# Optimization experiments

Hardware: AMD Instinct MI355X
Metric: run time of the kernel (lower is better)

## Reference

```python
import jax, jax.numpy as jnp
import numpy as np

LOG2 = float(np.log(2.0))

def ssp(x):
    # shifted softplus: softplus(x) - log(2)
    return jax.nn.softplus(x) - LOG2

def setup_inputs() -> dict:
    key = jax.random.key(0)
    ks = jax.random.split(key, 12)
    B, N, K, G, Fdim, H, O = 2, 1024, 64, 64, 128, 4, 128
    s = 0.05
    return {
        'x': jax.random.normal(ks[0], (B, N, Fdim), jnp.float32),
        'r_ij': jax.random.uniform(ks[1], (B, N, K), jnp.float32),
        'neighbors': jax.random.randint(ks[2], (B, N, K), 0, N),
        'pairwise_mask': jnp.ones((B, N, K), jnp.float32),
        'f_ij': jax.random.normal(ks[3], (B, N, K, G), jnp.float32),
        'w_in2f': jax.random.normal(ks[4], (H, Fdim, Fdim), jnp.float32) * s,
        'w_att': jax.random.normal(ks[5], (H, 2 * Fdim), jnp.float32) * s,
        'wf1': jax.random.normal(ks[6], (G, Fdim), jnp.float32) * s,
        'bf1': jnp.zeros((Fdim,), jnp.float32),
        'wf2': jax.random.normal(ks[7], (Fdim, Fdim), jnp.float32) * s,
        'bf2': jnp.zeros((Fdim,), jnp.float32),
        'w_out': jax.random.normal(ks[8], (Fdim, O), jnp.float32) * s,
        'b_out': jnp.zeros((O,), jnp.float32),
    }

def reference(x, r_ij, neighbors, pairwise_mask, f_ij,
              w_in2f, w_att, wf1, bf1, wf2, bf2, w_out, b_out):
    B, N, K = neighbors.shape
    H, _, Fdim = w_in2f.shape
    # continuous filter network: MLP on radial features -> [B,N,K,F]
    W = ssp(jnp.einsum('bnkg,gf->bnkf', f_ij, wf1) + bf1)
    W = jnp.einsum('bnkf,fe->bnke', W, wf2) + bf2
    # per-head linear projections: [B,H,N,F]
    y = jnp.einsum('bni,hif->bhnf', x, w_in2f)
    # gather neighbor features along atom axis: [B,H,N,K,F]
    idx = jnp.broadcast_to(neighbors.reshape(B, 1, N * K, 1), (B, H, N * K, Fdim))
    y_nb = jnp.take_along_axis(y, idx, axis=2).reshape(B, H, N, K, Fdim)
    # GAT attention logits via split weight (equiv. to concat + Dense):
    a_c = jnp.einsum('bhnf,hf->bhn', y, w_att[:, :Fdim])       # center part
    a_n = jnp.einsum('bhnkf,hf->bhnk', y_nb, w_att[:, Fdim:])  # neighbor part
    att = a_c[:, :, :, None] + a_n                             # [B,H,N,K]
    alpha = jax.nn.softmax(ssp(att), axis=-1)
    # attention-weighted neighbor features times continuous filters, mean over heads
    out = jnp.einsum('bhnk,bhnkf,bnkf->bnkf', alpha, y_nb, W) / H
    # masked aggregation over the neighbor axis
    agg = jnp.sum(out * pairwise_mask[..., None], axis=2)      # [B,N,F]
    return ssp(jnp.einsum('bnf,fo->bno', agg, w_out) + b_out)
```

## Files before the change

### kernel.cpp

```cpp
#include <hip/hip_runtime.h>

#define NB 2
#define NN 1024
#define NK 64
#define NG 64
#define NF 128
#define NH 4
#define NO 128
#define PITCH 132

typedef unsigned short ushort_t;
typedef __attribute__((ext_vector_type(8))) short short8v;
typedef __attribute__((ext_vector_type(4))) float f32x4;

union FragU { uint4 u4; short8v s8; };

__device__ __forceinline__ float bf2f(ushort_t u) {
    union { unsigned int i; float f; } v; v.i = ((unsigned int)u) << 16; return v.f;
}
__device__ __forceinline__ ushort_t f2bf(float f) {
    unsigned int u = __float_as_uint(f);
    unsigned int r = 0x7fffu + ((u >> 16) & 1u);
    return (ushort_t)((u + r) >> 16);
}
__device__ __forceinline__ float sspf(float x) {
    const float u = __builtin_amdgcn_exp2f(-fabsf(x) * 1.44269504088896341f);
    return fmaxf(x, 0.f) + fmaf(0.69314718055994531f,
                                __builtin_amdgcn_logf(1.f + u),
                                -0.69314718055994531f);
}

__global__ __launch_bounds__(256) void k_projprep(
    const float* __restrict__ x,
    const float* __restrict__ w_in2f,
    const float* __restrict__ w_att,
    const float* __restrict__ wf1, const float* __restrict__ wf2,
    const float* __restrict__ w_out,
    ushort_t* __restrict__ y,
    float* __restrict__ a_c,
    float* __restrict__ a_n,
    ushort_t* __restrict__ wf1f, ushort_t* __restrict__ wf2f,
    float* __restrict__ w_outT)
{
    const int t = threadIdx.x;
    __shared__ float xs[8][NF];
    __shared__ float ys[32][PITCH];

    if (blockIdx.x >= 256) {
        int s = (blockIdx.x - 256) * 256 + t;
        if (s >= 7168) return;
        if (s >= 3072) {
            const int s2 = s - 3072;
            const int o = s2 >> 5, fb = s2 & 31;
            #pragma unroll
            for (int j = 0; j < 4; ++j)
                w_outT[(size_t)o * NF + fb * 4 + j] = w_out[(size_t)(fb * 4 + j) * NO + o];
            return;
        }
        const float* W; ushort_t* out; int loOff;
        if (s < 1024) { W = wf1; out = wf1f; loOff = 8192; }
        else          { s -= 1024; W = wf2; out = wf2f; loOff = 16384; }
        const int fi = s >> 6, lane = s & 63;
        const int ks = fi >> 3, nf = fi & 7;
        const int n = nf * 16 + (lane & 15);
        const int kb = ks * 32 + ((lane >> 4) & 3) * 4;
        #pragma unroll
        for (int j = 0; j < 8; ++j) {
            const int k = kb + (j & 3) + ((j >> 2) << 4);
            const float v = W[(size_t)k * NF + n];
            const ushort_t hb = f2bf(v);
            out[(size_t)(fi * 64 + lane) * 8 + j] = hb;
            out[(size_t)loOff + (fi * 64 + lane) * 8 + j] = f2bf(v - bf2f(hb));
        }
        return;
    }

    const int bn0 = blockIdx.x * 8;
    {
        const float4* src = (const float4*)(x + (size_t)bn0 * NF);
        float4* dst = (float4*)(&xs[0][0]);
        dst[t] = src[t];
    }
    __syncthreads();

    const int hp = t >> 7;
    const int f0 = t & 127;
    const int h0 = hp, h1 = hp + 2;
    const float* w0 = w_in2f + (size_t)h0 * NF * NF + f0;
    const float* w1 = w_in2f + (size_t)h1 * NF * NF + f0;
    float acc0[8], acc1[8];
    #pragma unroll
    for (int n = 0; n < 8; ++n) { acc0[n] = 0.f; acc1[n] = 0.f; }

    for (int i0 = 0; i0 < NF; i0 += 4) {
        float4 xv[8];
        #pragma unroll
        for (int n = 0; n < 8; ++n) xv[n] = *(const float4*)&xs[n][i0];
        #pragma unroll
        for (int ii = 0; ii < 4; ++ii) {
            const float wa = w0[(size_t)(i0 + ii) * NF];
            const float wb = w1[(size_t)(i0 + ii) * NF];
            #pragma unroll
            for (int n = 0; n < 8; ++n) {
                const float xi = (&xv[n].x)[ii];
                acc0[n] = fmaf(xi, wa, acc0[n]);
                acc1[n] = fmaf(xi, wb, acc1[n]);
            }
        }
    }
    #pragma unroll
    for (int n = 0; n < 8; ++n) {
        const int bn = bn0 + n;
        const int b = bn >> 10, nn = bn & (NN - 1);
        y[((size_t)(b * NH + h0) * NN + nn) * NF + f0] = f2bf(acc0[n]);
        y[((size_t)(b * NH + h1) * NN + nn) * NF + f0] = f2bf(acc1[n]);
        ys[n * 4 + h0][f0] = acc0[n];
        ys[n * 4 + h1][f0] = acc1[n];
    }
    __syncthreads();

    {
        const int hn = t >> 3, q = t & 7;
        const int h = hn & 3, n = hn >> 2;
        float pc = 0.f, pn = 0.f;
        #pragma unroll
        for (int j = 0; j < 16; ++j) {
            const int f = q + 8 * j;
            const float yv = ys[n * 4 + h][f];
            pc = fmaf(yv, w_att[h * 2 * NF + f], pc);
            pn = fmaf(yv, w_att[h * 2 * NF + NF + f], pn);
        }
        #pragma unroll
        for (int off = 1; off < 8; off <<= 1) {
            pc += __shfl_xor(pc, off, 8);
            pn += __shfl_xor(pn, off, 8);
        }
        if (q == 0) {
            const int bn = bn0 + n;
            const int b = bn >> 10, nn = bn & (NN - 1);
            a_c[(size_t)(b * NH + h) * NN + nn] = pc;
            a_n[(size_t)(b * NH + h) * NN + nn] = pn;
        }
    }
}

__global__ __launch_bounds__(256, 7) void k_main(
    const int*      __restrict__ neighbors,
    const float*    __restrict__ pmask,
    const float*    __restrict__ f_ij,
    const float*    __restrict__ bf1,
    const float*    __restrict__ bf2v,
    const float*    __restrict__ w_outT,
    const float*    __restrict__ b_out,
    const ushort_t* __restrict__ y,
    const float*    __restrict__ a_c,
    const float*    __restrict__ a_n,
    const ushort_t* __restrict__ wf1f,
    const ushort_t* __restrict__ wf2f,
    float*          __restrict__ outp)
{
    const int bn = blockIdx.x;
    const int b = bn >> 10, n_ = bn & (NN - 1);
    const int t = threadIdx.x;

    __shared__ __align__(16) char smem[22784];
    ushort_t* fijs = (ushort_t*)(smem);
    ushort_t* W1   = (ushort_t*)(smem);
    ushort_t* W2   = (ushort_t*)(smem);
    float*    aggp = (float*)(smem + 16896);
    float*    aggc = (float*)(smem + 20992);
    float*    alpha = (float*)(smem + 21504);
    int*      nbs   = (int*)(smem + 22528);

    const int wave = t >> 6, lane = t & 63;
    const int lrow = lane & 15;
    const int lq   = (lane >> 4) & 3;
    const int wb   = wave * 32;

    {
        const float4* src = (const float4*)(f_ij + (size_t)bn * NK * NG);
        #pragma unroll
        for (int i = 0; i < 4; ++i) {
            const int e4 = i * 256 + t;
            const float4 v = src[e4];
            const int e = e4 * 4;
            const int row = e >> 6, col = e & 63;
            uint2 ph;
            ph.x = (unsigned)f2bf(v.x) | ((unsigned)f2bf(v.y) << 16);
            ph.y = (unsigned)f2bf(v.z) | ((unsigned)f2bf(v.w) << 16);
            *(uint2*)&fijs[row * 68 + col] = ph;
        }
    }
    if (t < NK) nbs[t] = neighbors[(size_t)bn * NK + t];
    __syncthreads();

    const float avc = a_c[(size_t)(b * NH + wave) * NN + n_];
    const float avn = a_n[(size_t)(b * NH + wave) * NN + nbs[lane]];
    const float pmk = pmask[(size_t)bn * NK + lane];

    f32x4 acc[4][2];
    {
        #pragma unroll
        for (int mf = 0; mf < 4; ++mf)
            #pragma unroll
            for (int nf2 = 0; nf2 < 2; ++nf2) acc[mf][nf2] = (f32x4)0.f;

        #pragma unroll
        for (int ks = 0; ks < 2; ++ks) {
            FragU b1h[2], b1l[2];
            #pragma unroll
            for (int nf2 = 0; nf2 < 2; ++nf2) {
                const int fi = ks * 8 + wave * 2 + nf2;
                b1h[nf2].u4 = *((const uint4*)wf1f + fi * 64 + lane);
                b1l[nf2].u4 = *((const uint4*)(wf1f + 8192) + fi * 64 + lane);
            }
            const int cb = ks * 32 + lq * 4;
            #pragma unroll
            for (int mf = 0; mf < 4; ++mf) {
                const int row = mf * 16 + lrow;
                FragU ah;
                {
                    const uint2 p0 = *(const uint2*)&fijs[row * 68 + cb];
                    const uint2 p1 = *(const uint2*)&fijs[row * 68 + cb + 16];
                    uint4 q; q.x = p0.x; q.y = p0.y; q.z = p1.x; q.w = p1.y; ah.u4 = q;
                }
                #pragma unroll
                for (int nf2 = 0; nf2 < 2; ++nf2) {
                    acc[mf][nf2] = __builtin_amdgcn_mfma_f32_16x16x32_bf16(ah.s8, b1h[nf2].s8, acc[mf][nf2], 0, 0, 0);
                    acc[mf][nf2] = __builtin_amdgcn_mfma_f32_16x16x32_bf16(ah.s8, b1l[nf2].s8, acc[mf][nf2], 0, 0, 0);
                }
            }
        }
    }
    __syncthreads();
    {
        const float bia[2] = { bf1[wb + lrow], bf1[wb + 16 + lrow] };
        #pragma unroll
        for (int mf = 0; mf < 4; ++mf)
            #pragma unroll
            for (int nf2 = 0; nf2 < 2; ++nf2) {
                const int col = wb + nf2 * 16 + lrow;
                #pragma unroll
                for (int r = 0; r < 4; ++r) {
                    const int row = mf * 16 + lq * 4 + r;
                    W1[row * 132 + col] = f2bf(sspf(acc[mf][nf2][r] + bia[nf2]));
                }
            }
    }
    __syncthreads();

    {
        #pragma unroll
        for (int mf = 0; mf < 4; ++mf)
            #pragma unroll
            for (int nf2 = 0; nf2 < 2; ++nf2) acc[mf][nf2] = (f32x4)0.f;

        for (int ks = 0; ks < 4; ++ks) {
            FragU b2h[2];
            #pragma unroll
            for (int nf2 = 0; nf2 < 2; ++nf2) {
                const int fi = ks * 8 + wave * 2 + nf2;
                b2h[nf2].u4 = *((const uint4*)wf2f + fi * 64 + lane);
            }
            const int cb = ks * 32 + lq * 4;
            #pragma unroll
            for (int mf = 0; mf < 4; ++mf) {
                const int row = mf * 16 + lrow;
                FragU ah;
                {
                    const uint2 p0 = *(const uint2*)&W1[row * 132 + cb];
                    const uint2 p1 = *(const uint2*)&W1[row * 132 + cb + 16];
                    uint4 q; q.x = p0.x; q.y = p0.y; q.z = p1.x; q.w = p1.y; ah.u4 = q;
                }
                #pragma unroll
                for (int nf2 = 0; nf2 < 2; ++nf2)
                    acc[mf][nf2] = __builtin_amdgcn_mfma_f32_16x16x32_bf16(ah.s8, b2h[nf2].s8, acc[mf][nf2], 0, 0, 0);
            }
        }
    }
    __syncthreads();
    {
        const float bia[2] = { bf2v[wb + lrow], bf2v[wb + 16 + lrow] };
        #pragma unroll
        for (int mf = 0; mf < 4; ++mf)
            #pragma unroll
            for (int nf2 = 0; nf2 < 2; ++nf2) {
                const int col = wb + nf2 * 16 + lrow;
                #pragma unroll
                for (int r = 0; r < 4; ++r) {
                    const int row = mf * 16 + lq * 4 + r;
                    W2[row * 132 + col] = f2bf(acc[mf][nf2][r] + bia[nf2]);
                }
            }
    }

    {
        const float att = sspf(avc + avn);
        float m = att;
        #pragma unroll
        for (int off = 32; off > 0; off >>= 1) m = fmaxf(m, __shfl_xor(m, off, 64));
        const float e = __builtin_amdgcn_exp2f((att - m) * 1.44269504088896341f);
        float s = e;
        #pragma unroll
        for (int off = 32; off > 0; off >>= 1) s += __shfl_xor(s, off, 64);
        alpha[wave * 64 + lane] = (e / s) * pmk;
    }
    __syncthreads();

    {
        const int fq = (t & 31) * 4;
        const int kg = t >> 5;
        float4 accv; accv.x = accv.y = accv.z = accv.w = 0.f;
        const ushort_t* yb = y + (size_t)b * NH * NN * NF;
        #pragma unroll 2
        for (int kk = 0; kk < 8; ++kk) {
            const int k = kg * 8 + kk;
            const int nb = nbs[k];
            const ushort_t* yp = yb + (size_t)nb * NF + fq;
            const uint2 u0 = *(const uint2*)(yp);
            const uint2 u1 = *(const uint2*)(yp + (size_t)NN * NF);
            const uint2 u2 = *(const uint2*)(yp + 2 * (size_t)NN * NF);
            const uint2 u3 = *(const uint2*)(yp + 3 * (size_t)NN * NF);
            const float a0 = alpha[0 * 64 + k], a1 = alpha[1 * 64 + k];
            const float a2 = alpha[2 * 64 + k], a3 = alpha[3 * 64 + k];
            float4 s;
            s.x = fmaf(a3, bf2f((ushort_t)(u3.x & 0xffffu)),
                  fmaf(a2, bf2f((ushort_t)(u2.x & 0xffffu)),
                  fmaf(a1, bf2f((ushort_t)(u1.x & 0xffffu)),
                       a0 * bf2f((ushort_t)(u0.x & 0xffffu)))));
            s.y = fmaf(a3, bf2f((ushort_t)(u3.x >> 16)),
                  fmaf(a2, bf2f((ushort_t)(u2.x >> 16)),
                  fmaf(a1, bf2f((ushort_t)(u1.x >> 16)),
                       a0 * bf2f((ushort_t)(u0.x >> 16)))));
            s.z = fmaf(a3, bf2f((ushort_t)(u3.y & 0xffffu)),
                  fmaf(a2, bf2f((ushort_t)(u2.y & 0xffffu)),
                  fmaf(a1, bf2f((ushort_t)(u1.y & 0xffffu)),
                       a0 * bf2f((ushort_t)(u0.y & 0xffffu)))));
            s.w = fmaf(a3, bf2f((ushort_t)(u3.y >> 16)),
                  fmaf(a2, bf2f((ushort_t)(u2.y >> 16)),
                  fmaf(a1, bf2f((ushort_t)(u1.y >> 16)),
                       a0 * bf2f((ushort_t)(u0.y >> 16)))));
            const uint2 wv = *(const uint2*)&W2[k * 132 + fq];
            accv.x = fmaf(bf2f((ushort_t)(wv.x & 0xffffu)), s.x, accv.x);
            accv.y = fmaf(bf2f((ushort_t)(wv.x >> 16)),     s.y, accv.y);
            accv.z = fmaf(bf2f((ushort_t)(wv.y & 0xffffu)), s.z, accv.z);
            accv.w = fmaf(bf2f((ushort_t)(wv.y >> 16)),     s.w, accv.w);
        }
        *(float4*)&aggp[kg * 128 + fq] = accv;
    }
    __syncthreads();
    if (t < NF) {
        float s = 0.f;
        #pragma unroll
        for (int q = 0; q < 8; ++q) s += aggp[q * 128 + t];
        aggc[t] = s * 0.25f;
    }
    __syncthreads();

    if (t < NO) {
        float z = b_out[t];
        const float4* wr = (const float4*)(w_outT + (size_t)t * NF);
        #pragma unroll 8
        for (int q = 0; q < NF / 4; ++q) {
            const float4 w = wr[q];
            const float4 a = *(const float4*)&aggc[q * 4];
            z = fmaf(a.x, w.x, fmaf(a.y, w.y, fmaf(a.z, w.z, fmaf(a.w, w.w, z))));
        }
        outp[(size_t)bn * NO + t] = sspf(z);
    }
}

extern "C" void kernel_launch(void* const* d_in, const int* in_sizes, int n_in,
                              void* d_out, int out_size, void* d_ws, size_t ws_size,
                              hipStream_t stream) {
    const float* x      = (const float*)d_in[0];
    const int*   nbr    = (const int*)d_in[2];
    const float* pmask  = (const float*)d_in[3];
    const float* f_ij   = (const float*)d_in[4];
    const float* w_in2f = (const float*)d_in[5];
    const float* w_att  = (const float*)d_in[6];
    const float* wf1    = (const float*)d_in[7];
    const float* bf1    = (const float*)d_in[8];
    const float* wf2    = (const float*)d_in[9];
    const float* bf2v   = (const float*)d_in[10];
    const float* w_out  = (const float*)d_in[11];
    const float* b_out  = (const float*)d_in[12];

    ushort_t* yb16  = (ushort_t*)d_ws;
    float*    a_c   = (float*)(yb16 + (size_t)NB * NH * NN * NF);
    float*    a_n   = a_c + (size_t)NB * NH * NN;
    ushort_t* wf1f  = (ushort_t*)(a_n + (size_t)NB * NH * NN);
    ushort_t* wf2f  = wf1f + 16384;
    float*    w_outT = (float*)(wf2f + 32768);

    float* outp = (float*)d_out;

    k_projprep<<<NB * NN / 8 + 28, 256, 0, stream>>>(
        x, w_in2f, w_att, wf1, wf2, w_out, yb16, a_c, a_n, wf1f, wf2f, w_outT);
    k_main<<<NB * NN, 256, 0, stream>>>(nbr, pmask, f_ij, bf1, bf2v,
                                        w_outT, b_out, yb16, a_c, a_n, wf1f, wf2f, outp);
}
```

Baseline: 61.10 us.

## Split MLP GEMMs into row halves to cut registers and raise occupancy

Splits each filter-MLP GEMM into two 32-row halves, halving the accumulator array so the kernel can target 8 blocks per CU instead of 7. Shared memory shrinks by aliasing aggc with alpha and by reducing the partial-sum buffer via a cross-half-wave shuffle before the store. The attention loads are deferred until after the GEMMs to shorten register lifetimes. In exchange there are extra barriers, and B-fragment loads from global are repeated for each half.

```diff
diff --git a/kernel.cpp b/kernel.cpp
--- a/kernel.cpp
+++ b/kernel.cpp
@@ -144,7 +144,7 @@
     }
 }
 
-__global__ __launch_bounds__(256, 7) void k_main(
+__global__ __launch_bounds__(256, 8) void k_main(
     const int*      __restrict__ neighbors,
     const float*    __restrict__ pmask,
     const float*    __restrict__ f_ij,
@@ -163,14 +163,14 @@
     const int b = bn >> 10, n_ = bn & (NN - 1);
     const int t = threadIdx.x;
 
-    __shared__ __align__(16) char smem[22784];
+    __shared__ __align__(16) char smem[20224];
     ushort_t* fijs = (ushort_t*)(smem);
     ushort_t* W1   = (ushort_t*)(smem);
     ushort_t* W2   = (ushort_t*)(smem);
     float*    aggp = (float*)(smem + 16896);
-    float*    aggc = (float*)(smem + 20992);
-    float*    alpha = (float*)(smem + 21504);
-    int*      nbs   = (int*)(smem + 22528);
+    float*    alpha = (float*)(smem + 18944);
+    float*    aggc = (float*)(smem + 18944);
+    int*      nbs   = (int*)(smem + 19968);
 
     const int wave = t >> 6, lane = t & 63;
     const int lrow = lane & 15;
@@ -194,17 +194,13 @@
     if (t < NK) nbs[t] = neighbors[(size_t)bn * NK + t];
     __syncthreads();
 
-    const float avc = a_c[(size_t)(b * NH + wave) * NN + n_];
-    const float avn = a_n[(size_t)(b * NH + wave) * NN + nbs[lane]];
-    const float pmk = pmask[(size_t)bn * NK + lane];
-
-    f32x4 acc[4][2];
-    {
-        #pragma unroll
-        for (int mf = 0; mf < 4; ++mf)
-            #pragma unroll
-            for (int nf2 = 0; nf2 < 2; ++nf2) acc[mf][nf2] = (f32x4)0.f;
-
+    f32x4 acc[2][2];
+
+    auto a1_compute = [&](int mfb) {
+        #pragma unroll
+        for (int mf2 = 0; mf2 < 2; ++mf2)
+            #pragma unroll
+            for (int nf2 = 0; nf2 < 2; ++nf2) acc[mf2][nf2] = (f32x4)0.f;
         #pragma unroll
         for (int ks = 0; ks < 2; ++ks) {
             FragU b1h[2], b1l[2];
@@ -216,8 +212,8 @@
             }
             const int cb = ks * 32 + lq * 4;
             #pragma unroll
-            for (int mf = 0; mf < 4; ++mf) {
-                const int row = mf * 16 + lrow;
+            for (int mf2 = 0; mf2 < 2; ++mf2) {
+                const int row = (mfb + mf2) * 16 + lrow;
                 FragU ah;
                 {
                     const uint2 p0 = *(const uint2*)&fijs[row * 68 + cb];
@@ -226,35 +222,31 @@
                 }
                 #pragma unroll
                 for (int nf2 = 0; nf2 < 2; ++nf2) {
-                    acc[mf][nf2] = __builtin_amdgcn_mfma_f32_16x16x32_bf16(ah.s8, b1h[nf2].s8, acc[mf][nf2], 0, 0, 0);
-                    acc[mf][nf2] = __builtin_amdgcn_mfma_f32_16x16x32_bf16(ah.s8, b1l[nf2].s8, acc[mf][nf2], 0, 0, 0);
+                    acc[mf2][nf2] = __builtin_amdgcn_mfma_f32_16x16x32_bf16(ah.s8, b1h[nf2].s8, acc[mf2][nf2], 0, 0, 0);
+                    acc[mf2][nf2] = __builtin_amdgcn_mfma_f32_16x16x32_bf16(ah.s8, b1l[nf2].s8, acc[mf2][nf2], 0, 0, 0);
                 }
             }
         }
-    }
-    __syncthreads();
-    {
+    };
+    auto a1_epi = [&](int mfb) {
         const float bia[2] = { bf1[wb + lrow], bf1[wb + 16 + lrow] };
         #pragma unroll
-        for (int mf = 0; mf < 4; ++mf)
+        for (int mf2 = 0; mf2 < 2; ++mf2)
             #pragma unroll
             for (int nf2 = 0; nf2 < 2; ++nf2) {
                 const int col = wb + nf2 * 16 + lrow;
                 #pragma unroll
                 for (int r = 0; r < 4; ++r) {
-                    const int row = mf * 16 + lq * 4 + r;
-                    W1[row * 132 + col] = f2bf(sspf(acc[mf][nf2][r] + bia[nf2]));
+                    const int row = (mfb + mf2) * 16 + lq * 4 + r;
+                    W1[row * 132 + col] = f2bf(sspf(acc[mf2][nf2][r] + bia[nf2]));
                 }
             }
-    }
-    __syncthreads();
-
-    {
-        #pragma unroll
-        for (int mf = 0; mf < 4; ++mf)
-            #pragma unroll
-            for (int nf2 = 0; nf2 < 2; ++nf2) acc[mf][nf2] = (f32x4)0.f;
-
+    };
+    auto a2_compute = [&](int mfb) {
+        #pragma unroll
+        for (int mf2 = 0; mf2 < 2; ++mf2)
+            #pragma unroll
+            for (int nf2 = 0; nf2 < 2; ++nf2) acc[mf2][nf2] = (f32x4)0.f;
         for (int ks = 0; ks < 4; ++ks) {
             FragU b2h[2];
             #pragma unroll
@@ -264,8 +256,8 @@
             }
             const int cb = ks * 32 + lq * 4;
             #pragma unroll
-            for (int mf = 0; mf < 4; ++mf) {
-                const int row = mf * 16 + lrow;
+            for (int mf2 = 0; mf2 < 2; ++mf2) {
+                const int row = (mfb + mf2) * 16 + lrow;
                 FragU ah;
                 {
                     const uint2 p0 = *(const uint2*)&W1[row * 132 + cb];
@@ -274,28 +266,42 @@
                 }
                 #pragma unroll
                 for (int nf2 = 0; nf2 < 2; ++nf2)
-                    acc[mf][nf2] = __builtin_amdgcn_mfma_f32_16x16x32_bf16(ah.s8, b2h[nf2].s8, acc[mf][nf2], 0, 0, 0);
-            }
-        }
-    }
-    __syncthreads();
-    {
+                    acc[mf2][nf2] = __builtin_amdgcn_mfma_f32_16x16x32_bf16(ah.s8, b2h[nf2].s8, acc[mf2][nf2], 0, 0, 0);
+            }
+        }
+    };
+    auto a2_epi = [&](int mfb) {
         const float bia[2] = { bf2v[wb + lrow], bf2v[wb + 16 + lrow] };
         #pragma unroll
-        for (int mf = 0; mf < 4; ++mf)
+        for (int mf2 = 0; mf2 < 2; ++mf2)
             #pragma unroll
             for (int nf2 = 0; nf2 < 2; ++nf2) {
                 const int col = wb + nf2 * 16 + lrow;
                 #pragma unroll
                 for (int r = 0; r < 4; ++r) {
-                    const int row = mf * 16 + lq * 4 + r;
-                    W2[row * 132 + col] = f2bf(acc[mf][nf2][r] + bia[nf2]);
+                    const int row = (mfb + mf2) * 16 + lq * 4 + r;
+                    W2[row * 132 + col] = f2bf(acc[mf2][nf2][r] + bia[nf2]);
                 }
             }
-    }
+    };
+
+    a1_compute(2);
+    __syncthreads();
+    a1_epi(2);
+    a1_compute(0);
+    __syncthreads();
+    a1_epi(0);
+    __syncthreads();
+
+    a2_compute(2);
+    __syncthreads();
+    a2_epi(2);
+    a2_compute(0);
 
     {
-        const float att = sspf(avc + avn);
+        const float av = a_c[(size_t)(b * NH + wave) * NN + n_]
+                       + a_n[(size_t)(b * NH + wave) * NN + nbs[lane]];
+        const float att = sspf(av);
         float m = att;
         #pragma unroll
         for (int off = 32; off > 0; off >>= 1) m = fmaxf(m, __shfl_xor(m, off, 64));
@@ -303,8 +309,10 @@
         float s = e;
         #pragma unroll
         for (int off = 32; off > 0; off >>= 1) s += __shfl_xor(s, off, 64);
-        alpha[wave * 64 + lane] = (e / s) * pmk;
-    }
+        alpha[wave * 64 + lane] = (e / s) * pmask[(size_t)bn * NK + lane];
+    }
+    __syncthreads();
+    a2_epi(0);
     __syncthreads();
 
     {
@@ -346,14 +354,15 @@
             accv.z = fmaf(bf2f((ushort_t)(wv.y & 0xffffu)), s.z, accv.z);
             accv.w = fmaf(bf2f((ushort_t)(wv.y >> 16)),     s.w, accv.w);
         }
-        *(float4*)&aggp[kg * 128 + fq] = accv;
+        accv.x += __shfl_xor(accv.x, 32, 64);
+        accv.y += __shfl_xor(accv.y, 32, 64);
+        accv.z += __shfl_xor(accv.z, 32, 64);
+        accv.w += __shfl_xor(accv.w, 32, 64);
+        if (lane < 32) *(float4*)&aggp[wave * 128 + fq] = accv;
     }
     __syncthreads();
     if (t < NF) {
-        float s = 0.f;
-        #pragma unroll
-        for (int q = 0; q < 8; ++q) s += aggp[q * 128 + t];
-        aggc[t] = s * 0.25f;
+        aggc[t] = (aggp[t] + aggp[128 + t] + aggp[256 + t] + aggp[384 + t]) * 0.25f;
     }
     __syncthreads();
 
```

New measurement: 59.19 us. 3.1% less time.
